# Performance work log

Hardware: AMD Instinct MI355X
Metric: run time of the kernel (lower is better)

The kernel has to match this reference:

```python
import jax, jax.numpy as jnp
import numpy as np
import math

B, Q, D, H = 256, 512, 32, 192
BLOCKS, KERNEL, EXPAND = 2, 9, 2
HID = H * EXPAND
IN_CH = 3 * D  # feature_mode='y_dy_ddy'


def _ln(x, w, b, eps=1e-5):
    m = x.mean(-1, keepdims=True)
    v = ((x - m) ** 2).mean(-1, keepdims=True)
    return (x - m) * jax.lax.rsqrt(v + eps) * w + b


def _features(x_in):
    # [y, dy, ddy] with dy[0]=0, ddy[0]=ddy[1 via diff]=...
    dy = jnp.concatenate([jnp.zeros_like(x_in[:, :1]), jnp.diff(x_in, axis=1)], axis=1)
    ddy = jnp.concatenate([jnp.zeros_like(dy[:, :1]), jnp.diff(dy, axis=1)], axis=1)
    return jnp.concatenate([x_in, dy, ddy], axis=-1)  # [B,Q,3D]


def _rotate(x, rho, phi):
    M = x.shape[-1] // 2
    re, im = x[:, :M], x[:, M:]
    c, s = jnp.cos(phi), jnp.sin(phi)
    return jnp.concatenate([rho * (c * re - s * im), rho * (s * re + c * im)], axis=1)


def _rho_phi(h2):
    return jax.nn.sigmoid(h2[:, 0:1]) * 1.25, math.pi * jnp.tanh(h2[:, 1:2])


def _block(h, dw_w, dw_b, ln_w, ln_b, pw1_w, pw1_b, grn_g, grn_b, pw2_w, pw2_b):
    # h: [B,C,T]; depthwise conv with replicate padding
    pad = KERNEL // 2
    y = jnp.pad(h, ((0, 0), (0, 0), (pad, pad)), mode='edge')
    y = jax.lax.conv_general_dilated(
        y, dw_w, (1,), 'VALID',
        dimension_numbers=('NCH', 'OIH', 'NCH'),
        feature_group_count=h.shape[1]) + dw_b[None, :, None]
    y = _ln(y.transpose(0, 2, 1), ln_w, ln_b).transpose(0, 2, 1)
    y = jnp.einsum('bct,oc->bot', y, pw1_w) + pw1_b[None, :, None]  # pw expand
    y = jax.nn.gelu(y, approximate=False)
    # GRN: L2 over time, normalize by channel-mean
    gx = jnp.sqrt(jnp.sum(y * y, axis=2, keepdims=True))  # [B,C,1]
    nx = gx / (gx.mean(axis=1, keepdims=True) + 1e-6)
    y = grn_g[None, :, None] * (y * nx) + grn_b[None, :, None] + y
    y = jnp.einsum('bct,oc->bot', y, pw2_w) + pw2_b[None, :, None]  # pw shrink
    return h + y  # dropout is identity in eval


def _forward(x_in, inp_w, inp_b, b_dw_w, b_dw_b, b_ln_w, b_ln_b,
             b_pw1_w, b_pw1_b, b_grn_g, b_grn_b, b_pw2_w, b_pw2_b,
             out_ln_w, out_ln_b, fc_rp_w, fc_rp_b, fc_gain_w, fc_gain_b,
             roll_in_w, roll_in_b, gru_wih, gru_whh, gru_bih, gru_bhh,
             roll_ln_w, roll_ln_b, fc_rp_r_w, fc_rp_r_b, w_out):
    feats = _features(x_in)  # [B,Q,3D]
    h = jnp.einsum('btc,oc->bot', feats, inp_w) + inp_b[None, :, None]  # [B,H,Q]
    for i in range(BLOCKS):
        h = _block(h, b_dw_w[i], b_dw_b[i], b_ln_w[i], b_ln_b[i],
                   b_pw1_w[i], b_pw1_b[i], b_grn_g[i], b_grn_b[i],
                   b_pw2_w[i], b_pw2_b[i])
    h_seq = _ln(h.transpose(0, 2, 1), out_ln_w, out_ln_b)  # [B,Q,H]

    # predict-correct Kalman loop (sequential over Q)
    def kstep(x_post, inp):
        h_t, y_t = inp
        rho, phi = _rho_phi(h_t @ fc_rp_w.T + fc_rp_b)
        x_pri = _rotate(x_post, rho, phi)
        gain = jax.nn.sigmoid(h_t @ fc_gain_w.T + fc_gain_b)
        return x_pri + gain * (y_t - x_pri), None

    x_post, _ = jax.lax.scan(
        kstep, x_in[:, 0, :],
        (h_seq.transpose(1, 0, 2), x_in.transpose(1, 0, 2)))

    # GRU rollout
    Hn = gru_whh.shape[1]

    def rstep(carry, _):
        h_r, curr = carry
        x = jnp.tanh(jnp.concatenate([h_r, curr], 1) @ roll_in_w.T + roll_in_b)
        gi = x @ gru_wih.T + gru_bih
        gh = h_r @ gru_whh.T + gru_bhh
        r = jax.nn.sigmoid(gi[:, :Hn] + gh[:, :Hn])
        z = jax.nn.sigmoid(gi[:, Hn:2 * Hn] + gh[:, Hn:2 * Hn])
        n = jnp.tanh(gi[:, 2 * Hn:] + r * gh[:, 2 * Hn:])
        h_new = _ln((1 - z) * n + z * h_r, roll_ln_w, roll_ln_b)
        rho, phi = _rho_phi(h_new @ fc_rp_r_w.T + fc_rp_r_b)
        curr_new = _rotate(curr, rho, phi)
        return (h_new, curr_new), curr_new

    _, preds = jax.lax.scan(rstep, (h_seq[:, -1, :], x_post), None, length=w_out)
    return preds.transpose(1, 0, 2)  # [B, w_out, D]


def setup_inputs() -> dict:
    key = jax.random.key(0)
    ks = jax.random.split(key, 32)
    n = lambda i, shape, s=0.05: jax.random.normal(ks[i], shape, jnp.float32) * s
    return {
        'x_in': jax.random.normal(ks[0], (B, Q, D), jnp.float32),
        'inp_w': n(1, (H, IN_CH)), 'inp_b': n(2, (H,)),
        'b_dw_w': n(3, (BLOCKS, H, 1, KERNEL)), 'b_dw_b': n(4, (BLOCKS, H)),
        'b_ln_w': 1.0 + n(5, (BLOCKS, H)), 'b_ln_b': n(6, (BLOCKS, H)),
        'b_pw1_w': n(7, (BLOCKS, HID, H)), 'b_pw1_b': n(8, (BLOCKS, HID)),
        'b_grn_g': n(9, (BLOCKS, HID)), 'b_grn_b': n(10, (BLOCKS, HID)),
        'b_pw2_w': n(11, (BLOCKS, H, HID)), 'b_pw2_b': n(12, (BLOCKS, H)),
        'out_ln_w': 1.0 + n(13, (H,)), 'out_ln_b': n(14, (H,)),
        'fc_rp_w': n(15, (2, H)), 'fc_rp_b': n(16, (2,)),
        'fc_gain_w': n(17, (D, H)), 'fc_gain_b': n(18, (D,)),
        'roll_in_w': n(19, (H, H + D)), 'roll_in_b': n(20, (H,)),
        'gru_wih': n(21, (3 * H, H)), 'gru_whh': n(22, (3 * H, H)),
        'gru_bih': n(23, (3 * H,)), 'gru_bhh': n(24, (3 * H,)),
        'roll_ln_w': 1.0 + n(25, (H,)), 'roll_ln_b': n(26, (H,)),
        'fc_rp_r_w': n(27, (2, H)), 'fc_rp_r_b': n(28, (2,)),
        'w_out': 64,
    }


def reference(x_in, inp_w, inp_b, b_dw_w, b_dw_b, b_ln_w, b_ln_b,
              b_pw1_w, b_pw1_b, b_grn_g, b_grn_b, b_pw2_w, b_pw2_b,
              out_ln_w, out_ln_b, fc_rp_w, fc_rp_b, fc_gain_w, fc_gain_b,
              roll_in_w, roll_in_b, gru_wih, gru_whh, gru_bih, gru_bhh,
              roll_ln_w, roll_ln_b, fc_rp_r_w, fc_rp_r_b, w_out):
    return _forward(x_in, inp_w, inp_b, b_dw_w, b_dw_b, b_ln_w, b_ln_b,
                    b_pw1_w, b_pw1_b, b_grn_g, b_grn_b, b_pw2_w, b_pw2_b,
                    out_ln_w, out_ln_b, fc_rp_w, fc_rp_b, fc_gain_w, fc_gain_b,
                    roll_in_w, roll_in_b, gru_wih, gru_whh, gru_bih, gru_bhh,
                    roll_ln_w, roll_ln_b, fc_rp_r_w, fc_rp_r_b, int(w_out))
```

## Files before the change

### kernel.cpp

```cpp
#include <hip/hip_runtime.h>
#include <cstdint>
#include <cstddef>

#define B_    256
#define Q_    512
#define D_    32
#define H_    192
#define HID_  384
#define INCH_ 96
#define M_    (B_*Q_)
#define WOUT_ 64
#define BPB   2
#define RT_   768
#define PI_F  3.14159265358979323846f
#define LDS_S 40

typedef unsigned int uint_t;
typedef __attribute__((ext_vector_type(8))) short short8v;
typedef __attribute__((ext_vector_type(4))) float floatx4;

__device__ __forceinline__ float sigm(float x){ return 1.f/(1.f+expf(-x)); }
__device__ __forceinline__ float gelu_exact(float x){ return 0.5f*x*(1.f+erff(x*0.7071067811865475f)); }
__device__ __forceinline__ float4 f4sub(float4 a, float4 b){
  return make_float4(a.x-b.x, a.y-b.y, a.z-b.z, a.w-b.w);
}

__device__ __forceinline__ void f2bf2(float v, unsigned short& h, unsigned short& l){
  unsigned u = __float_as_uint(v);
  unsigned rh = u + 0x7FFFu + ((u>>16)&1u);
  h = (unsigned short)(rh>>16);
  float fh = __uint_as_float(((unsigned)h)<<16);
  float lo = v - fh;
  unsigned ul = __float_as_uint(lo);
  unsigned rl = ul + 0x7FFFu + ((ul>>16)&1u);
  l = (unsigned short)(rl>>16);
}

#define MFMA_BF16(a,b,c) __builtin_amdgcn_mfma_f32_16x16x32_bf16((a),(b),(c),0,0,0)

__device__ __forceinline__ float4 feats_load(const float* __restrict__ x, int bt, int c){
  const int t = bt & 511;
  const int seg = c >> 5, d = c & 31;
  const float* xr = x + (size_t)bt*D_ + d;
  float4 x0 = *(const float4*)xr;
  if (seg == 0) return x0;
  if (t == 0) return make_float4(0.f,0.f,0.f,0.f);
  float4 x1 = *(const float4*)(xr - D_);
  float4 dy = f4sub(x0, x1);
  if (seg == 1) return dy;
  if (t == 1) return dy;
  float4 x2 = *(const float4*)(xr - 2*D_);
  float4 dym1 = f4sub(x1, x2);
  return f4sub(dy, dym1);
}

__global__ void prep_wbf_kernel(const float* __restrict__ w1, const float* __restrict__ w2,
                                unsigned short* __restrict__ w1h, unsigned short* __restrict__ w1l,
                                unsigned short* __restrict__ w2h, unsigned short* __restrict__ w2l)
{
  int idx = blockIdx.x*256 + threadIdx.x;
  const int n1 = 2*HID_*H_;
  if (idx < n1){
    unsigned short h,l; f2bf2(w1[idx],h,l);
    w1h[idx]=h; w1l[idx]=l;
    return;
  }
  idx -= n1;
  if (idx < 2*H_*HID_){
    unsigned short h,l; f2bf2(w2[idx],h,l);
    w2h[idx]=h; w2l[idx]=l;
  }
}

template<int MODE>
__global__ __launch_bounds__(256,2) void gemm_mfma(
    const float* __restrict__ Af, const unsigned* __restrict__ Ap,
    const unsigned short* __restrict__ Wh, const unsigned short* __restrict__ Wl,
    const float* __restrict__ bias,
    float* __restrict__ Cf,
    const float* __restrict__ scale, const float* __restrict__ grnb,
    float* __restrict__ gpart,
    int N, int K)
{
  __shared__ __align__(16) unsigned short smem[25600];
  unsigned short* Ah = smem;
  unsigned short* Al = smem + 128*LDS_S;
  unsigned short* Bh = smem + 256*LDS_S;
  unsigned short* Bl = smem + 256*LDS_S + 192*LDS_S;

  const int tid  = threadIdx.x;
  const int lane = tid & 63;
  const int wv   = tid >> 6;
  const int l15  = lane & 15;
  const int lg   = lane >> 4;
  const int bm = blockIdx.x*128, bn = blockIdx.y*192;

  floatx4 acc[2][12];
  #pragma unroll
  for (int i=0;i<2;i++)
    #pragma unroll
    for (int j=0;j<12;j++) acc[i][j] = (floatx4){0.f,0.f,0.f,0.f};

  const int arow = tid >> 1, akq = (tid & 1)*16;
  const float*    gA  = (MODE==2) ? (Af + (size_t)(bm+arow)*K) : nullptr;
  const unsigned* gAp = (MODE==1) ? (Ap + (size_t)(bm+arow)*K) : nullptr;
  const float* srow = (MODE==2) ? (scale + (size_t)(bm>>9)*HID_) : nullptr;

  for (int k0=0; k0<K; k0+=32){
    if (MODE==1){
      #pragma unroll
      for (int i=0;i<4;i++){
        uint4 u = *(const uint4*)(gAp + k0 + akq + 4*i);
        unsigned h01 = (u.x & 0xFFFFu) | (u.y << 16);
        unsigned h23 = (u.z & 0xFFFFu) | (u.w << 16);
        unsigned l01 = (u.x >> 16) | (u.y & 0xFFFF0000u);
        unsigned l23 = (u.z >> 16) | (u.w & 0xFFFF0000u);
        uint2 uh; uh.x=h01; uh.y=h23;
        uint2 ul; ul.x=l01; ul.y=l23;
        *(uint2*)&Ah[arow*LDS_S + akq + 4*i] = uh;
        *(uint2*)&Al[arow*LDS_S + akq + 4*i] = ul;
      }
    } else {
      #pragma unroll
      for (int i=0;i<4;i++){
        float4 v = *(const float4*)(gA + k0 + akq + 4*i);
        int c = k0 + akq + 4*i;
        float4 sc = *(const float4*)(srow+c);
        float4 gb = *(const float4*)(grnb+c);
        v.x = v.x*sc.x+gb.x; v.y = v.y*sc.y+gb.y;
        v.z = v.z*sc.z+gb.z; v.w = v.w*sc.w+gb.w;
        unsigned short h0,h1,h2,h3,l0,l1,l2,l3;
        f2bf2(v.x,h0,l0); f2bf2(v.y,h1,l1); f2bf2(v.z,h2,l2); f2bf2(v.w,h3,l3);
        uint2 uh; uh.x = (unsigned)h0 | ((unsigned)h1<<16); uh.y = (unsigned)h2 | ((unsigned)h3<<16);
        uint2 ul; ul.x = (unsigned)l0 | ((unsigned)l1<<16); ul.y = (unsigned)l2 | ((unsigned)l3<<16);
        *(uint2*)&Ah[arow*LDS_S + akq + 4*i] = uh;
        *(uint2*)&Al[arow*LDS_S + akq + 4*i] = ul;
      }
    }
    for (int idx = tid; idx < 384; idx += 256){
      int br = idx >> 1, bkq = (idx & 1)*16;
      const unsigned short* gh = Wh + (size_t)(bn+br)*K + k0 + bkq;
      const unsigned short* gl = Wl + (size_t)(bn+br)*K + k0 + bkq;
      uint4 vh0 = *(const uint4*)(gh);
      uint4 vh1 = *(const uint4*)(gh+8);
      uint4 vl0 = *(const uint4*)(gl);
      uint4 vl1 = *(const uint4*)(gl+8);
      *(uint4*)&Bh[br*LDS_S + bkq]     = vh0;
      *(uint4*)&Bh[br*LDS_S + bkq + 8] = vh1;
      *(uint4*)&Bl[br*LDS_S + bkq]     = vl0;
      *(uint4*)&Bl[br*LDS_S + bkq + 8] = vl1;
    }
    __syncthreads();

    const int a0off = (wv*32 + l15)*LDS_S + 8*lg;
    const int a1off = a0off + 16*LDS_S;
    short8v ah0 = *(const short8v*)&Ah[a0off];
    short8v al0 = *(const short8v*)&Al[a0off];
    short8v ah1 = *(const short8v*)&Ah[a1off];
    short8v al1 = *(const short8v*)&Al[a1off];
    #pragma unroll
    for (int ct=0; ct<12; ct++){
      const int boff = (ct*16 + l15)*LDS_S + 8*lg;
      short8v bh = *(const short8v*)&Bh[boff];
      short8v bl = *(const short8v*)&Bl[boff];
      acc[0][ct] = MFMA_BF16(ah0, bh, acc[0][ct]);
      acc[0][ct] = MFMA_BF16(ah0, bl, acc[0][ct]);
      acc[0][ct] = MFMA_BF16(al0, bh, acc[0][ct]);
      acc[1][ct] = MFMA_BF16(ah1, bh, acc[1][ct]);
      acc[1][ct] = MFMA_BF16(ah1, bl, acc[1][ct]);
      acc[1][ct] = MFMA_BF16(al1, bh, acc[1][ct]);
    }
    __syncthreads();
  }

  if (MODE==1){
    float* gq = (float*)smem;
    #pragma unroll
    for (int ct=0; ct<12; ct++){
      const int col = bn + ct*16 + l15;
      const float b = bias[col];
      float qc = 0.f;
      #pragma unroll
      for (int rt=0; rt<2; rt++){
        const int rbase = bm + wv*32 + rt*16 + lg*4;
        #pragma unroll
        for (int r=0;r<4;r++){
          float v = gelu_exact(acc[rt][ct][r] + b);
          Cf[(size_t)(rbase+r)*N + col] = v;
          qc += v*v;
        }
      }
      gq[(ct*16+l15)*16 + (wv*4+lg)] = qc;
    }
    __syncthreads();
    if (tid < 192){
      float s = 0.f;
      #pragma unroll
      for (int j=0;j<16;j++) s += gq[tid*16+j];
      const int slot = (bm>>7)&3, b = bm>>9;
      gpart[((size_t)(b*4+slot))*HID_ + bn + tid] = s;
    }
  } else {
    #pragma unroll
    for (int ct=0; ct<12; ct++){
      const int col = bn + ct*16 + l15;
      const float b = bias[col];
      #pragma unroll
      for (int rt=0; rt<2; rt++){
        const int rbase = bm + wv*32 + rt*16 + lg*4;
        #pragma unroll
        for (int r=0;r<4;r++){
          size_t off = (size_t)(rbase+r)*N + col;
          Cf[off] = Cf[off] + acc[rt][ct][r] + b;
        }
      }
    }
  }
}

__global__ __launch_bounds__(256,2) void gemm_inp_w192(
    const float* __restrict__ x,
    const float* __restrict__ W,  const float* __restrict__ bias,
    float* __restrict__ Cf)
{
  __shared__ float smem[16*128 + 16*192];
  float* AsB = smem;
  float* BsB = smem + 16*128;
  const int tid = threadIdx.x;
  const int bm = blockIdx.x*128;
  const int tx = tid & 15, ty = tid >> 4;
  const int arow = tid >> 1, ak = (tid & 1)*4;
  const int br = tid >> 2,  bk = (tid & 3)*4;
  const int K = INCH_, N = H_;

  float acc[8][12];
  #pragma unroll
  for (int i=0;i<8;i++)
    #pragma unroll
    for (int j=0;j<12;j++) acc[i][j]=0.f;

  const float* gB0 = W + (size_t)(br)*K;
  const float* gB1 = W + (size_t)(br+64)*K;
  const float* gB2 = W + (size_t)(br+128)*K;

  for (int k0=0;k0<K;k0+=16){
    float4 va0 = feats_load(x, bm+arow, k0+ak);
    float4 va1 = feats_load(x, bm+arow, k0+ak+8);
    float4 vb0 = *(const float4*)(gB0 + k0 + bk);
    float4 vb1 = *(const float4*)(gB1 + k0 + bk);
    float4 vb2 = *(const float4*)(gB2 + k0 + bk);
    AsB[(ak+0)*128+arow]=va0.x; AsB[(ak+1)*128+arow]=va0.y; AsB[(ak+2)*128+arow]=va0.z; AsB[(ak+3)*128+arow]=va0.w;
    AsB[(ak+8)*128+arow]=va1.x; AsB[(ak+9)*128+arow]=va1.y; AsB[(ak+10)*128+arow]=va1.z; AsB[(ak+11)*128+arow]=va1.w;
    BsB[(bk+0)*192+br]=vb0.x; BsB[(bk+1)*192+br]=vb0.y; BsB[(bk+2)*192+br]=vb0.z; BsB[(bk+3)*192+br]=vb0.w;
    BsB[(bk+0)*192+br+64]=vb1.x; BsB[(bk+1)*192+br+64]=vb1.y; BsB[(bk+2)*192+br+64]=vb1.z; BsB[(bk+3)*192+br+64]=vb1.w;
    BsB[(bk+0)*192+br+128]=vb2.x; BsB[(bk+1)*192+br+128]=vb2.y; BsB[(bk+2)*192+br+128]=vb2.z; BsB[(bk+3)*192+br+128]=vb2.w;
    __syncthreads();
    #pragma unroll
    for (int kk=0;kk<16;kk++){
      float4 a0 = *(const float4*)&AsB[kk*128 + ty*8];
      float4 a1 = *(const float4*)&AsB[kk*128 + ty*8 + 4];
      float4 b0 = *(const float4*)&BsB[kk*192 + tx*12];
      float4 b1 = *(const float4*)&BsB[kk*192 + tx*12 + 4];
      float4 b2 = *(const float4*)&BsB[kk*192 + tx*12 + 8];
      float ar[8] = {a0.x,a0.y,a0.z,a0.w,a1.x,a1.y,a1.z,a1.w};
      #pragma unroll
      for (int i=0;i<8;i++){
        acc[i][0] += ar[i]*b0.x; acc[i][1] += ar[i]*b0.y; acc[i][2] += ar[i]*b0.z; acc[i][3] += ar[i]*b0.w;
        acc[i][4] += ar[i]*b1.x; acc[i][5] += ar[i]*b1.y; acc[i][6] += ar[i]*b1.z; acc[i][7] += ar[i]*b1.w;
        acc[i][8] += ar[i]*b2.x; acc[i][9] += ar[i]*b2.y; acc[i][10]+= ar[i]*b2.z; acc[i][11]+= ar[i]*b2.w;
      }
    }
    __syncthreads();
  }

  const int o0 = tx*12;
  float4 bb0 = *(const float4*)(bias + o0);
  float4 bb1 = *(const float4*)(bias + o0 + 4);
  float4 bb2 = *(const float4*)(bias + o0 + 8);
  #pragma unroll
  for (int i=0;i<8;i++){
    int m = bm + ty*8 + i;
    float* crow = Cf + (size_t)m*N + o0;
    float4 v0, v1, v2;
    v0.x=acc[i][0]+bb0.x; v0.y=acc[i][1]+bb0.y; v0.z=acc[i][2]+bb0.z; v0.w=acc[i][3]+bb0.w;
    v1.x=acc[i][4]+bb1.x; v1.y=acc[i][5]+bb1.y; v1.z=acc[i][6]+bb1.z; v1.w=acc[i][7]+bb1.w;
    v2.x=acc[i][8]+bb2.x; v2.y=acc[i][9]+bb2.y; v2.z=acc[i][10]+bb2.z; v2.w=acc[i][11]+bb2.w;
    *(float4*)(crow+0) = v0; *(float4*)(crow+4) = v1; *(float4*)(crow+8) = v2;
  }
}

template<int MODE>
__global__ __launch_bounds__(256,4) void gemm_t128(
    const float* __restrict__ Af,
    const float* __restrict__ W,  const float* __restrict__ bias,
    float* __restrict__ Cf,
    const float* __restrict__ scale, const float* __restrict__ grnb,
    float* __restrict__ gpart,
    int N, int K)
{
  __shared__ float As[16][128];
  __shared__ float Bs[16][64];
  const int tid = threadIdx.x;
  const int bm = blockIdx.x*128, bn = blockIdx.y*64;
  const int tx = tid & 15, ty = tid >> 4;
  const int arow = tid >> 1, ak = (tid & 1)*4;
  const int brow = tid >> 2, bk = (tid & 3)*4;

  float acc[8][4];
  #pragma unroll
  for (int i=0;i<8;i++)
    #pragma unroll
    for (int j=0;j<4;j++) acc[i][j]=0.f;

  const float* gA = Af + (size_t)(bm+arow)*K;
  const float* gB = W  + (size_t)(bn+brow)*K;

  for (int k0=0;k0<K;k0+=16){
    float4 va0 = *(const float4*)(gA + k0 + ak);
    float4 va1 = *(const float4*)(gA + k0 + ak + 8);
    float4 vb  = *(const float4*)(gB + k0 + bk);
    As[ak+0][arow]=va0.x; As[ak+1][arow]=va0.y; As[ak+2][arow]=va0.z; As[ak+3][arow]=va0.w;
    As[ak+8][arow]=va1.x; As[ak+9][arow]=va1.y; As[ak+10][arow]=va1.z; As[ak+11][arow]=va1.w;
    Bs[bk+0][brow]=vb.x; Bs[bk+1][brow]=vb.y; Bs[bk+2][brow]=vb.z; Bs[bk+3][brow]=vb.w;
    __syncthreads();
    #pragma unroll
    for (int kk=0;kk<16;kk++){
      float4 a0 = *(const float4*)&As[kk][ty*8];
      float4 a1 = *(const float4*)&As[kk][ty*8+4];
      float4 b  = *(const float4*)&Bs[kk][tx*4];
      float ar[8] = {a0.x,a0.y,a0.z,a0.w,a1.x,a1.y,a1.z,a1.w};
      #pragma unroll
      for (int i=0;i<8;i++){
        acc[i][0] += ar[i]*b.x; acc[i][1] += ar[i]*b.y;
        acc[i][2] += ar[i]*b.z; acc[i][3] += ar[i]*b.w;
      }
    }
    __syncthreads();
  }

  const int o0 = bn + tx*4;
  float4 b0 = *(const float4*)(bias + o0);

  if (MODE==3){
    #pragma unroll
    for (int i=0;i<8;i++){
      int m = bm + ty*8 + i;
      float* ob = Cf + (size_t)m*34;
      float vx = acc[i][0]+b0.x, vy = acc[i][1]+b0.y;
      float vz = acc[i][2]+b0.z, vw = acc[i][3]+b0.w;
      if (o0 == 0){
        float rho = 1.25f*sigm(vx);
        float phi = PI_F*tanhf(vy);
        ob[0] = rho*cosf(phi); ob[1] = rho*sinf(phi);
        ob[2] = sigm(vz); ob[3] = sigm(vw);
      } else if (o0 <= 28){
        ob[o0+0]=sigm(vx); ob[o0+1]=sigm(vy); ob[o0+2]=sigm(vz); ob[o0+3]=sigm(vw);
      } else if (o0 == 32){
        ob[32]=sigm(vx); ob[33]=sigm(vy);
      }
    }
    return;
  }
  (void)gpart; (void)scale; (void)grnb;
}

__global__ __launch_bounds__(256) void dwconv_ln_wave(
  const float* __restrict__ h, const float* __restrict__ dww, const float* __restrict__ dwb,
  const float* __restrict__ lnw, const float* __restrict__ lnb, unsigned* __restrict__ yln)
{
  __shared__ float sh[24][192];
  const int tid  = threadIdx.x;
  const int lane = tid & 63;
  const int wv   = tid >> 6;
  const int t0 = (blockIdx.x & 31) * 16;
  const size_t base = (size_t)(blockIdx.x >> 5) * Q_ * H_;
  #pragma unroll
  for (int i = tid; i < 24*192; i += 256){
    int r = i / 192, c = i - r*192;
    int tt = t0 - 4 + r; tt = tt<0?0:(tt>511?511:tt);
    sh[r][c] = h[base + (size_t)tt*H_ + c];
  }
  const int c0 = lane, c1 = lane+64, c2 = lane+128;
  float w0[9], w1[9], w2[9];
  #pragma unroll
  for (int k=0;k<9;k++){ w0[k]=dww[c0*9+k]; w1[k]=dww[c1*9+k]; w2[k]=dww[c2*9+k]; }
  const float db0=dwb[c0], db1=dwb[c1], db2=dwb[c2];
  const float lw0=lnw[c0], lw1=lnw[c1], lw2=lnw[c2];
  const float lb0=lnb[c0], lb1=lnb[c1], lb2=lnb[c2];
  __syncthreads();
  for (int it=0; it<4; it++){
    const int i = it*4 + wv;
    float a0=db0, a1=db1, a2=db2;
    #pragma unroll
    for (int k=0;k<9;k++){
      a0 += w0[k]*sh[i+k][c0];
      a1 += w1[k]*sh[i+k][c1];
      a2 += w2[k]*sh[i+k][c2];
    }
    float s = a0+a1+a2;
    float qq = a0*a0 + a1*a1 + a2*a2;
    #pragma unroll
    for (int off=32; off>0; off>>=1){ s += __shfl_down(s,off); qq += __shfl_down(qq,off); }
    s = __shfl(s, 0); qq = __shfl(qq, 0);
    float mean = s*(1.f/H_);
    float var  = qq*(1.f/H_) - mean*mean;
    float r = rsqrtf(var + 1e-5f);
    unsigned* ob = yln + base + (size_t)(t0+i)*H_;
    unsigned short hh,ll;
    f2bf2((a0-mean)*r*lw0 + lb0, hh, ll); ob[c0] = (unsigned)hh | ((unsigned)ll<<16);
    f2bf2((a1-mean)*r*lw1 + lb1, hh, ll); ob[c1] = (unsigned)hh | ((unsigned)ll<<16);
    f2bf2((a2-mean)*r*lw2 + lb2, hh, ll); ob[c2] = (unsigned)hh | ((unsigned)ll<<16);
  }
}

__global__ __launch_bounds__(256) void out_ln_wave(
  const float* __restrict__ h, const float* __restrict__ lnw, const float* __restrict__ lnb,
  float* __restrict__ o, float* __restrict__ hlast, int b0)
{
  const int tid  = threadIdx.x;
  const int lane = tid & 63;
  const int wv   = tid >> 6;
  const int bt = blockIdx.x*4 + wv;
  const float* hr = h + (size_t)bt*H_;
  float v0 = hr[lane], v1 = hr[lane+64], v2 = hr[lane+128];
  float s = v0+v1+v2;
  float qq = v0*v0 + v1*v1 + v2*v2;
  #pragma unroll
  for (int off=32; off>0; off>>=1){ s += __shfl_down(s,off); qq += __shfl_down(qq,off); }
  s = __shfl(s, 0); qq = __shfl(qq, 0);
  float mean = s*(1.f/H_);
  float var  = qq*(1.f/H_) - mean*mean;
  float r = rsqrtf(var + 1e-5f);
  const float r0 = (v0-mean)*r*lnw[lane]     + lnb[lane];
  const float r1 = (v1-mean)*r*lnw[lane+64]  + lnb[lane+64];
  const float r2 = (v2-mean)*r*lnw[lane+128] + lnb[lane+128];
  float* orow = o + (size_t)bt*H_;
  orow[lane] = r0; orow[lane+64] = r1; orow[lane+128] = r2;
  if ((bt & 511) == 511){
    float* hl = hlast + (size_t)(b0 + (bt>>9))*H_;
    hl[lane] = r0; hl[lane+64] = r1; hl[lane+128] = r2;
  }
}

__global__ __launch_bounds__(384) void grn_combine_kernel(
  const float* __restrict__ gpart, const float* __restrict__ grn_g, float* __restrict__ scale)
{
  __shared__ float r[384];
  const int c = threadIdx.x;
  const int b = blockIdx.x;
  const float* p = gpart + (size_t)b*4*HID_;
  float s = ((p[c] + p[HID_+c]) + p[2*HID_+c]) + p[3*HID_+c];
  float gx = sqrtf(s);
  r[c] = gx;
  __syncthreads();
  if (c < 64){
    float v = r[c]+r[c+64]+r[c+128]+r[c+192]+r[c+256]+r[c+320];
    #pragma unroll
    for (int off=32; off>0; off>>=1) v += __shfl_down(v,off);
    if (c==0) r[0]=v;
  }
  __syncthreads();
  float mean = r[0]*(1.f/HID_);
  scale[(size_t)b*HID_ + c] = 1.f + grn_g[c]*gx/(mean + 1e-6f);
}

__global__ void pack_w_kernel(const float* __restrict__ frw, const float* __restrict__ frb,
                              const float* __restrict__ fgw, const float* __restrict__ fgb,
                              float* __restrict__ w_pad, float* __restrict__ b_pad)
{
  int idx = blockIdx.x*256 + threadIdx.x;
  if (idx >= 64*192) return;
  int o = idx / 192, k = idx % 192;
  float v = 0.f;
  if (o < 2) v = frw[o*192+k]; else if (o < 34) v = fgw[(o-2)*192+k];
  w_pad[idx] = v;
  if (k == 0){
    float bv = 0.f;
    if (o < 2) bv = frb[o]; else if (o < 34) bv = fgb[o-2];
    b_pad[o] = bv;
  }
}

__global__ __launch_bounds__(64) void kalman_scan_kernel(
  const float* __restrict__ x_c, const float* __restrict__ rp, float* __restrict__ xpost,
  int b0, int Bc)
{
  const int lane = threadIdx.x;
  const int bl = blockIdx.x*4 + (lane>>4);
  if (bl >= Bc) return;
  const int m = lane & 15;
  const float* xb  = x_c + (size_t)bl*Q_*D_;
  const float* rpb = rp  + (size_t)bl*Q_*34;
  float re = xb[m], im = xb[16+m];
  for (int t=0;t<Q_;t++){
    const float* r = rpb + (size_t)t*34;
    float rc = r[0], rs = r[1];
    float g0 = r[2+m], g1 = r[18+m];
    float y0 = xb[(size_t)t*D_ + m], y1v = xb[(size_t)t*D_ + 16 + m];
    float pr  = rc*re - rs*im;
    float pim = rs*re + rc*im;
    re = pr  + g0*(y0  - pr);
    im = pim + g1*(y1v - pim);
  }
  xpost[(b0+bl)*D_ + m] = re;
  xpost[(b0+bl)*D_ + 16 + m] = im;
}

__global__ void prep_rollout_kernel(const float* __restrict__ riw, const float* __restrict__ wih,
                                    const float* __restrict__ whh,
                                    float* __restrict__ wT1, float* __restrict__ wPack)
{
  int idx = blockIdx.x*256 + threadIdx.x;
  if (idx < 224*192){
    int o = idx % 192, k = idx / 192;
    wT1[idx] = riw[o*224 + k];
    return;
  }
  idx -= 224*192;
  if (idx < 192*192){
    int o = idx % 192, k = idx / 192;
    float* w = wPack + ((size_t)(k>>1)*192 + o)*12 + (k&1)*6;
    w[0] = wih[(0*192+o)*192 + k];
    w[1] = wih[(1*192+o)*192 + k];
    w[2] = wih[(2*192+o)*192 + k];
    w[3] = whh[(0*192+o)*192 + k];
    w[4] = whh[(1*192+o)*192 + k];
    w[5] = whh[(2*192+o)*192 + k];
  }
}

__global__ __launch_bounds__(RT_,3) void rollout_kernel(
  const float* __restrict__ hlast, const float* __restrict__ xpost,
  const float* __restrict__ wT1,  const float* __restrict__ rib_,
  const float* __restrict__ wPack,
  const float* __restrict__ bih,  const float* __restrict__ bhh,
  const float* __restrict__ lnw,  const float* __restrict__ lnb,
  const float* __restrict__ frw,  const float* __restrict__ frb,
  float* __restrict__ out)
{
  const int tid = threadIdx.x;
  const int q   = tid / 192;
  const int o   = tid - q*192;
  const int bb  = blockIdx.x*BPB;

  __shared__ float hT[192][2];
  __shared__ float xT[192][2];
  __shared__ float cT[32][2];
  __shared__ float pA[4][2][192];
  __shared__ float pB[4][12][192];
  __shared__ float rsum[2][3][4];

  if (q < 2){
    hT[o][q] = hlast[(size_t)(bb+q)*H_ + o];
    if (o < 32) cT[o][q] = xpost[(bb+q)*D_ + o];
  }

  const float w_ln = lnw[o], b_ln = lnb[o];
  const float fr0  = frw[o], fr1  = frw[192+o];
  const float fb0 = frb[0],  fb1 = frb[1];
  const float bi0 = bih[o], bi1 = bih[192+o], bi2 = bih[384+o];
  const float bh0 = bhh[o], bh1 = bhh[192+o], bh2 = bhh[384+o];
  const float rib = rib_[o];
  const float u0 = w_ln*fr0, u1 = w_ln*fr1;
  const float t0c = b_ln*fr0, t1c = b_ln*fr1;

  float wreg[56];
  if (q < 3){
    const int kb = 56*q;
    #pragma unroll
    for (int i=0;i<56;i++) wreg[i] = wT1[(kb+i)*192+o];
  } else {
    #pragma unroll
    for (int i=0;i<24;i++) wreg[i] = wT1[(168+i)*192+o];
    #pragma unroll
    for (int i=0;i<32;i++) wreg[24+i] = wT1[(192+i)*192+o];
  }

  {
    float c0=u0, c1=u1, k0=t0c, k1=t1c;
    #pragma unroll
    for (int off=32; off>0; off>>=1){
      c0 += __shfl_down(c0,off); c1 += __shfl_down(c1,off);
      k0 += __shfl_down(k0,off); k1 += __shfl_down(k1,off);
    }
    if (q==0 && (o&63)==0){
      int w = o>>6;
      rsum[0][w][0]=c0; rsum[0][w][1]=c1; rsum[0][w][2]=k0; rsum[0][w][3]=k1;
    }
  }
  __syncthreads();
  const float C0 = rsum[0][0][0]+rsum[0][1][0]+rsum[0][2][0];
  const float C1 = rsum[0][0][1]+rsum[0][1][1]+rsum[0][2][1];
  const float K0 = rsum[0][0][2]+rsum[0][1][2]+rsum[0][2][2] + fb0;
  const float K1 = rsum[0][0][3]+rsum[0][1][3]+rsum[0][2][3] + fb1;

  for (int s=0; s<WOUT_; s++){
    float a0=0.f, a1=0.f;
    if (q < 3){
      const int kb = 56*q;
      #pragma unroll
      for (int i=0;i<56;i++){
        float2 h2 = *(const float2*)&hT[kb+i][0];
        a0 += wreg[i]*h2.x; a1 += wreg[i]*h2.y;
      }
    } else {
      #pragma unroll
      for (int i=0;i<24;i++){
        float2 h2 = *(const float2*)&hT[168+i][0];
        a0 += wreg[i]*h2.x; a1 += wreg[i]*h2.y;
      }
      #pragma unroll
      for (int i=0;i<32;i++){
        float2 c2 = *(const float2*)&cT[i][0];
        a0 += wreg[24+i]*c2.x; a1 += wreg[24+i]*c2.y;
      }
    }
    pA[q][0][o]=a0; pA[q][1][o]=a1;
    __syncthreads();

    if (q < 2){
      xT[o][q] = tanhf(rib + pA[0][q][o] + pA[1][q][o] + pA[2][q][o] + pA[3][q][o]);
    }
    __syncthreads();

    float accx[2][3] = {{0.f,0.f,0.f},{0.f,0.f,0.f}};
    float acch[2][3] = {{0.f,0.f,0.f},{0.f,0.f,0.f}};
    {
      const int pb = 24*q;
      #pragma unroll 2
      for (int i=0;i<24;i++){
        const int p = pb+i;
        const float4* wp = (const float4*)(wPack + ((size_t)p*192 + o)*12);
        const float4 qa = wp[0];
        const float4 qb = wp[1];
        const float4 qc = wp[2];
        const float4 xx = *(const float4*)&xT[2*p][0];
        const float4 hh = *(const float4*)&hT[2*p][0];
        accx[0][0] += qa.x*xx.x; accx[0][1] += qa.y*xx.x; accx[0][2] += qa.z*xx.x;
        accx[1][0] += qa.x*xx.y; accx[1][1] += qa.y*xx.y; accx[1][2] += qa.z*xx.y;
        acch[0][0] += qa.w*hh.x; acch[0][1] += qb.x*hh.x; acch[0][2] += qb.y*hh.x;
        acch[1][0] += qa.w*hh.y; acch[1][1] += qb.x*hh.y; acch[1][2] += qb.y*hh.y;
        accx[0][0] += qb.z*xx.z; accx[0][1] += qb.w*xx.z; accx[0][2] += qc.x*xx.z;
        accx[1][0] += qb.z*xx.w; accx[1][1] += qb.w*xx.w; accx[1][2] += qc.x*xx.w;
        acch[0][0] += qc.y*hh.z; acch[0][1] += qc.z*hh.z; acch[0][2] += qc.w*hh.z;
        acch[1][0] += qc.y*hh.w; acch[1][1] += qc.z*hh.w; acch[1][2] += qc.w*hh.w;
      }
    }
    #pragma unroll
    for (int j=0;j<2;j++){
      #pragma unroll
      for (int g=0;g<3;g++){
        pB[q][j*6+g][o]   = accx[j][g];
        pB[q][j*6+3+g][o] = acch[j][g];
      }
    }
    __syncthreads();

    float pre = 0.f;
    if (q < 2){
      const int g6 = q*6;
      float P0 = bi0 + pB[0][g6+0][o]+pB[1][g6+0][o]+pB[2][g6+0][o]+pB[3][g6+0][o];
      float P1 = bi1 + pB[0][g6+1][o]+pB[1][g6+1][o]+pB[2][g6+1][o]+pB[3][g6+1][o];
      float P2 = bi2 + pB[0][g6+2][o]+pB[1][g6+2][o]+pB[2][g6+2][o]+pB[3][g6+2][o];
      float Q0 = bh0 + pB[0][g6+3][o]+pB[1][g6+3][o]+pB[2][g6+3][o]+pB[3][g6+3][o];
      float Q1 = bh1 + pB[0][g6+4][o]+pB[1][g6+4][o]+pB[2][g6+4][o]+pB[3][g6+4][o];
      float Q2 = bh2 + pB[0][g6+5][o]+pB[1][g6+5][o]+pB[2][g6+5][o]+pB[3][g6+5][o];
      float rg = sigm(P0+Q0), zz = sigm(P1+Q1);
      float nn = tanhf(P2 + rg*Q2);
      pre = (1.f-zz)*nn + zz*hT[o][q];
      float s1 = pre, s2 = pre*pre, s3 = pre*u0, s4 = pre*u1;
      #pragma unroll
      for (int off=32; off>0; off>>=1){
        s1 += __shfl_down(s1,off); s2 += __shfl_down(s2,off);
        s3 += __shfl_down(s3,off); s4 += __shfl_down(s4,off);
      }
      if ((o&63)==0){
        int w = o>>6;
        rsum[q][w][0]=s1; rsum[q][w][1]=s2; rsum[q][w][2]=s3; rsum[q][w][3]=s4;
      }
    }
    __syncthreads();

    if (q < 2){
      float S1 = rsum[q][0][0]+rsum[q][1][0]+rsum[q][2][0];
      float S2 = rsum[q][0][1]+rsum[q][1][1]+rsum[q][2][1];
      float mu  = S1*(1.f/192.f);
      float var = S2*(1.f/192.f) - mu*mu;
      float r = rsqrtf(var+1e-5f);
      hT[o][q] = (pre-mu)*r*w_ln + b_ln;
    } else if (o < 16){
      const int j = q-2;
      float S1 = rsum[j][0][0]+rsum[j][1][0]+rsum[j][2][0];
      float S2 = rsum[j][0][1]+rsum[j][1][1]+rsum[j][2][1];
      float S3 = rsum[j][0][2]+rsum[j][1][2]+rsum[j][2][2];
      float S4 = rsum[j][0][3]+rsum[j][1][3]+rsum[j][2][3];
      float mu  = S1*(1.f/192.f);
      float var = S2*(1.f/192.f) - mu*mu;
      float r = rsqrtf(var+1e-5f);
      float proj0 = r*(S3 - mu*C0) + K0;
      float proj1 = r*(S4 - mu*C1) + K1;
      float rho = 1.25f*sigm(proj0);
      float phi = PI_F*tanhf(proj1);
      float rc = rho*cosf(phi), rs = rho*sinf(phi);
      float re = cT[o][j], im = cT[o+16][j];
      float nre = rc*re - rs*im;
      float nim = rs*re + rc*im;
      cT[o][j] = nre; cT[o+16][j] = nim;
      float* ob = out + ((size_t)(bb+j)*WOUT_ + s)*D_;
      ob[o] = nre; ob[o+16] = nim;
    }
    __syncthreads();
  }
}

extern "C" void kernel_launch(void* const* d_in, const int* in_sizes, int n_in,
                              void* d_out, int out_size, void* d_ws, size_t ws_size,
                              hipStream_t stream)
{
  const float* x_in     = (const float*)d_in[0];
  const float* inp_w    = (const float*)d_in[1];
  const float* inp_b    = (const float*)d_in[2];
  const float* b_dw_w   = (const float*)d_in[3];
  const float* b_dw_b   = (const float*)d_in[4];
  const float* b_ln_w   = (const float*)d_in[5];
  const float* b_ln_b   = (const float*)d_in[6];
  const float* b_pw1_w  = (const float*)d_in[7];
  const float* b_pw1_b  = (const float*)d_in[8];
  const float* b_grn_g  = (const float*)d_in[9];
  const float* b_grn_b  = (const float*)d_in[10];
  const float* b_pw2_w  = (const float*)d_in[11];
  const float* b_pw2_b  = (const float*)d_in[12];
  const float* out_ln_w = (const float*)d_in[13];
  const float* out_ln_b = (const float*)d_in[14];
  const float* fc_rp_w  = (const float*)d_in[15];
  const float* fc_rp_b  = (const float*)d_in[16];
  const float* fc_gain_w= (const float*)d_in[17];
  const float* fc_gain_b= (const float*)d_in[18];
  const float* roll_in_w= (const float*)d_in[19];
  const float* roll_in_b= (const float*)d_in[20];
  const float* gru_wih  = (const float*)d_in[21];
  const float* gru_whh  = (const float*)d_in[22];
  const float* gru_bih  = (const float*)d_in[23];
  const float* gru_bhh  = (const float*)d_in[24];
  const float* roll_ln_w= (const float*)d_in[25];
  const float* roll_ln_b= (const float*)d_in[26];
  const float* fc_rp_r_w= (const float*)d_in[27];
  const float* fc_rp_r_b= (const float*)d_in[28];
  float* out = (float*)d_out;

  const size_t SMAL_FLOATS = 1194048 + 4096;
  size_t ws_floats = ws_size / 4;
  int nchunk = 256;
  const int cand[9] = {1,2,4,8,16,32,64,128,256};
  for (int ci=0; ci<9; ci++){
    size_t Mc_try = (size_t)M_ / cand[ci];
    if (Mc_try*768 + SMAL_FLOATS <= ws_floats){ nchunk = cand[ci]; break; }
  }
  const int    Bc = B_ / nchunk;
  const size_t Mc = (size_t)Bc * Q_;

  float* ws    = (float*)d_ws;
  float* h_c   = ws;
  float* yln_c = h_c   + Mc*192;
  float* mid_c = yln_c + Mc*192;
  float* smal  = mid_c + Mc*384;

  float* y1_c    = mid_c;
  float* rp_c    = mid_c;

  float* scaleB = smal;
  float* w_pad  = smal + 98304;
  float* b_pad  = w_pad + 12288;
  float* xpost  = b_pad + 64;
  float* hlast  = xpost + 8192;
  float* wT1    = hlast + 49152;
  float* wPack  = wT1 + 43008;
  float* gpart  = wPack + 294912;
  float* wbf    = gpart + 393216;
  unsigned short* w1h = (unsigned short*)wbf;
  unsigned short* w1l = w1h + 2*HID_*H_;
  unsigned short* w2h = w1l + 2*HID_*H_;
  unsigned short* w2l = w2h + 2*H_*HID_;

  pack_w_kernel<<<(64*192+255)/256, 256, 0, stream>>>(fc_rp_w, fc_rp_b, fc_gain_w, fc_gain_b, w_pad, b_pad);
  prep_rollout_kernel<<<(224*192+192*192+255)/256, 256, 0, stream>>>(roll_in_w, gru_wih, gru_whh, wT1, wPack);
  prep_wbf_kernel<<<(4*HID_*H_+255)/256, 256, 0, stream>>>(b_pw1_w, b_pw2_w, w1h, w1l, w2h, w2l);

  const int gmx = (int)(Mc/128);
  for (int ch=0; ch<nchunk; ch++){
    const float* x_c = x_in + (size_t)ch*Mc*D_;
    gemm_inp_w192<<<dim3(gmx, 1), 256, 0, stream>>>(x_c, inp_w, inp_b, h_c);
    for (int blk = 0; blk < 2; blk++){
      const float* dww = b_dw_w + blk*H_*9;     const float* dwb = b_dw_b + blk*H_;
      const float* lnw = b_ln_w + blk*H_;       const float* lnb = b_ln_b + blk*H_;
      const float* p1b = b_pw1_b + blk*HID_;
      const float* gg  = b_grn_g + blk*HID_;    const float* gb  = b_grn_b + blk*HID_;
      const float* p2b = b_pw2_b + blk*H_;
      dwconv_ln_wave<<<(int)(Mc/16), 256, 0, stream>>>(h_c, dww, dwb, lnw, lnb, (unsigned*)yln_c);
      gemm_mfma<1><<<dim3(gmx, 2), 256, 0, stream>>>(nullptr, (const unsigned*)yln_c,
                                                     w1h + blk*HID_*H_, w1l + blk*HID_*H_, p1b,
                                                     y1_c, nullptr, nullptr, gpart, HID_, H_);
      grn_combine_kernel<<<Bc, 384, 0, stream>>>(gpart, gg, scaleB);
      gemm_mfma<2><<<dim3(gmx, 1), 256, 0, stream>>>(y1_c, nullptr,
                                                     w2h + blk*H_*HID_, w2l + blk*H_*HID_, p2b,
                                                     h_c, scaleB, gb, nullptr, H_, HID_);
    }
    out_ln_wave<<<(int)(Mc/4), 256, 0, stream>>>(h_c, out_ln_w, out_ln_b, yln_c, hlast, ch*Bc);
    gemm_t128<3><<<dim3(gmx, 1), 256, 0, stream>>>(yln_c, w_pad, b_pad,
                                                   rp_c, nullptr, nullptr, nullptr, 64, H_);
    kalman_scan_kernel<<<(Bc+3)/4, 64, 0, stream>>>(x_c, rp_c, xpost, ch*Bc, Bc);
  }
  rollout_kernel<<<B_/BPB, RT_, 0, stream>>>(hlast, xpost, wT1, roll_in_b, wPack,
                                             gru_bih, gru_bhh, roll_ln_w, roll_ln_b,
                                             fc_rp_r_w, fc_rp_r_b, out);
  (void)in_sizes; (void)n_in; (void)out_size; (void)ws_size;
}
```

Baseline: 1.889 ms.

## Move output projection to MFMA, fuse GRN combine, widen dwconv tile

Replaces the fp32 SIMT projection GEMM with a bf16 hi/lo split MFMA kernel. To feed it, the output LayerNorm now writes packed bf16 pairs and the projection weights are converted once up front. The GRN scale computation is folded into the start of the second pointwise GEMM, removing a launch and a global round trip. The depthwise conv tile grows from 16 to 32 timesteps per block, which cuts halo reloads but halves the grid. Together these aim to reduce launch count and fp32 FMA work, at the cost of redundant per-block GRN reductions and three-product bf16 approximation error.

```diff
diff --git a/kernel.cpp b/kernel.cpp
--- a/kernel.cpp
+++ b/kernel.cpp
@@ -72,17 +72,27 @@
   }
 }
 
+__global__ void prep_wpad_bf(const float* __restrict__ wp,
+                             unsigned short* __restrict__ ph, unsigned short* __restrict__ pl)
+{
+  int idx = blockIdx.x*256 + threadIdx.x;
+  if (idx >= 64*192) return;
+  unsigned short h,l; f2bf2(wp[idx],h,l);
+  ph[idx]=h; pl[idx]=l;
+}
+
 template<int MODE>
 __global__ __launch_bounds__(256,2) void gemm_mfma(
     const float* __restrict__ Af, const unsigned* __restrict__ Ap,
     const unsigned short* __restrict__ Wh, const unsigned short* __restrict__ Wl,
     const float* __restrict__ bias,
     float* __restrict__ Cf,
-    const float* __restrict__ scale, const float* __restrict__ grnb,
+    const float* __restrict__ grn_g, const float* __restrict__ grnb,
     float* __restrict__ gpart,
     int N, int K)
 {
   __shared__ __align__(16) unsigned short smem[25600];
+  __shared__ float scLDS[HID_];
   unsigned short* Ah = smem;
   unsigned short* Al = smem + 128*LDS_S;
   unsigned short* Bh = smem + 256*LDS_S;
@@ -95,6 +105,29 @@
   const int lg   = lane >> 4;
   const int bm = blockIdx.x*128, bn = blockIdx.y*192;
 
+  if (MODE==2){
+    float* gx = (float*)smem;
+    const int b = bm>>9;
+    const float* p = gpart + (size_t)b*4*HID_;
+    for (int c=tid; c<HID_; c+=256){
+      float s = ((p[c] + p[HID_+c]) + p[2*HID_+c]) + p[3*HID_+c];
+      gx[c] = sqrtf(s);
+    }
+    __syncthreads();
+    if (tid < 64){
+      float v = gx[tid]+gx[tid+64]+gx[tid+128]+gx[tid+192]+gx[tid+256]+gx[tid+320];
+      #pragma unroll
+      for (int off=32; off>0; off>>=1) v += __shfl_down(v,off);
+      if (tid==0) gx[400] = v;
+    }
+    __syncthreads();
+    const float mean = gx[400]*(1.f/HID_);
+    for (int c=tid; c<HID_; c+=256){
+      scLDS[c] = 1.f + grn_g[c]*gx[c]/(mean + 1e-6f);
+    }
+    __syncthreads();
+  }
+
   floatx4 acc[2][12];
   #pragma unroll
   for (int i=0;i<2;i++)
@@ -104,7 +137,6 @@
   const int arow = tid >> 1, akq = (tid & 1)*16;
   const float*    gA  = (MODE==2) ? (Af + (size_t)(bm+arow)*K) : nullptr;
   const unsigned* gAp = (MODE==1) ? (Ap + (size_t)(bm+arow)*K) : nullptr;
-  const float* srow = (MODE==2) ? (scale + (size_t)(bm>>9)*HID_) : nullptr;
 
   for (int k0=0; k0<K; k0+=32){
     if (MODE==1){
@@ -125,7 +157,7 @@
       for (int i=0;i<4;i++){
         float4 v = *(const float4*)(gA + k0 + akq + 4*i);
         int c = k0 + akq + 4*i;
-        float4 sc = *(const float4*)(srow+c);
+        float4 sc = *(const float4*)&scLDS[c];
         float4 gb = *(const float4*)(grnb+c);
         v.x = v.x*sc.x+gb.x; v.y = v.y*sc.y+gb.y;
         v.z = v.z*sc.z+gb.z; v.w = v.w*sc.w+gb.w;
@@ -212,6 +244,113 @@
         for (int r=0;r<4;r++){
           size_t off = (size_t)(rbase+r)*N + col;
           Cf[off] = Cf[off] + acc[rt][ct][r] + b;
+        }
+      }
+    }
+  }
+}
+
+__global__ __launch_bounds__(256,2) void gemm_mfma_proj(
+    const unsigned* __restrict__ Ap,
+    const unsigned short* __restrict__ Wh, const unsigned short* __restrict__ Wl,
+    const float* __restrict__ bias,
+    float* __restrict__ rp)
+{
+  __shared__ __align__(16) unsigned short smem[15360];
+  unsigned short* Ah = smem;
+  unsigned short* Al = smem + 128*LDS_S;
+  unsigned short* Bh = smem + 256*LDS_S;
+  unsigned short* Bl = smem + 256*LDS_S + 64*LDS_S;
+  const int K = H_;
+
+  const int tid  = threadIdx.x;
+  const int lane = tid & 63;
+  const int wv   = tid >> 6;
+  const int l15  = lane & 15;
+  const int lg   = lane >> 4;
+  const int bm = blockIdx.x*128;
+
+  floatx4 acc[2][4];
+  #pragma unroll
+  for (int i=0;i<2;i++)
+    #pragma unroll
+    for (int j=0;j<4;j++) acc[i][j] = (floatx4){0.f,0.f,0.f,0.f};
+
+  const int arow = tid >> 1, akq = (tid & 1)*16;
+  const unsigned* gAp = Ap + (size_t)(bm+arow)*K;
+
+  for (int k0=0; k0<K; k0+=32){
+    #pragma unroll
+    for (int i=0;i<4;i++){
+      uint4 u = *(const uint4*)(gAp + k0 + akq + 4*i);
+      unsigned h01 = (u.x & 0xFFFFu) | (u.y << 16);
+      unsigned h23 = (u.z & 0xFFFFu) | (u.w << 16);
+      unsigned l01 = (u.x >> 16) | (u.y & 0xFFFF0000u);
+      unsigned l23 = (u.z >> 16) | (u.w & 0xFFFF0000u);
+      uint2 uh; uh.x=h01; uh.y=h23;
+      uint2 ul; ul.x=l01; ul.y=l23;
+      *(uint2*)&Ah[arow*LDS_S + akq + 4*i] = uh;
+      *(uint2*)&Al[arow*LDS_S + akq + 4*i] = ul;
+    }
+    if (tid < 128){
+      int br = tid >> 1, bkq = (tid & 1)*16;
+      const unsigned short* gh = Wh + (size_t)br*K + k0 + bkq;
+      const unsigned short* gl = Wl + (size_t)br*K + k0 + bkq;
+      uint4 vh0 = *(const uint4*)(gh);
+      uint4 vh1 = *(const uint4*)(gh+8);
+      uint4 vl0 = *(const uint4*)(gl);
+      uint4 vl1 = *(const uint4*)(gl+8);
+      *(uint4*)&Bh[br*LDS_S + bkq]     = vh0;
+      *(uint4*)&Bh[br*LDS_S + bkq + 8] = vh1;
+      *(uint4*)&Bl[br*LDS_S + bkq]     = vl0;
+      *(uint4*)&Bl[br*LDS_S + bkq + 8] = vl1;
+    }
+    __syncthreads();
+
+    const int a0off = (wv*32 + l15)*LDS_S + 8*lg;
+    const int a1off = a0off + 16*LDS_S;
+    short8v ah0 = *(const short8v*)&Ah[a0off];
+    short8v al0 = *(const short8v*)&Al[a0off];
+    short8v ah1 = *(const short8v*)&Ah[a1off];
+    short8v al1 = *(const short8v*)&Al[a1off];
+    #pragma unroll
+    for (int ct=0; ct<4; ct++){
+      const int boff = (ct*16 + l15)*LDS_S + 8*lg;
+      short8v bh = *(const short8v*)&Bh[boff];
+      short8v bl = *(const short8v*)&Bl[boff];
+      acc[0][ct] = MFMA_BF16(ah0, bh, acc[0][ct]);
+      acc[0][ct] = MFMA_BF16(ah0, bl, acc[0][ct]);
+      acc[0][ct] = MFMA_BF16(al0, bh, acc[0][ct]);
+      acc[1][ct] = MFMA_BF16(ah1, bh, acc[1][ct]);
+      acc[1][ct] = MFMA_BF16(ah1, bl, acc[1][ct]);
+      acc[1][ct] = MFMA_BF16(al1, bh, acc[1][ct]);
+    }
+    __syncthreads();
+  }
+
+  #pragma unroll
+  for (int ct=0; ct<4; ct++){
+    const int c = ct*16 + l15;
+    const float b = bias[c];
+    #pragma unroll
+    for (int rt=0; rt<2; rt++){
+      const int rbase = bm + wv*32 + rt*16 + lg*4;
+      #pragma unroll
+      for (int r=0;r<4;r++){
+        float val = acc[rt][ct][r] + b;
+        float* ob = rp + (size_t)(rbase+r)*34;
+        if (ct == 0){
+          float vn = __shfl(val, lane+1);
+          if (l15 == 0){
+            float rho = 1.25f*sigm(val);
+            float phi = PI_F*tanhf(vn);
+            ob[0] = rho*cosf(phi);
+            ob[1] = rho*sinf(phi);
+          } else if (c >= 2){
+            ob[c] = sigm(val);
+          }
+        } else if (c <= 33){
+          ob[c] = sigm(val);
         }
       }
     }
@@ -289,93 +428,17 @@
   }
 }
 
-template<int MODE>
-__global__ __launch_bounds__(256,4) void gemm_t128(
-    const float* __restrict__ Af,
-    const float* __restrict__ W,  const float* __restrict__ bias,
-    float* __restrict__ Cf,
-    const float* __restrict__ scale, const float* __restrict__ grnb,
-    float* __restrict__ gpart,
-    int N, int K)
-{
-  __shared__ float As[16][128];
-  __shared__ float Bs[16][64];
-  const int tid = threadIdx.x;
-  const int bm = blockIdx.x*128, bn = blockIdx.y*64;
-  const int tx = tid & 15, ty = tid >> 4;
-  const int arow = tid >> 1, ak = (tid & 1)*4;
-  const int brow = tid >> 2, bk = (tid & 3)*4;
-
-  float acc[8][4];
-  #pragma unroll
-  for (int i=0;i<8;i++)
-    #pragma unroll
-    for (int j=0;j<4;j++) acc[i][j]=0.f;
-
-  const float* gA = Af + (size_t)(bm+arow)*K;
-  const float* gB = W  + (size_t)(bn+brow)*K;
-
-  for (int k0=0;k0<K;k0+=16){
-    float4 va0 = *(const float4*)(gA + k0 + ak);
-    float4 va1 = *(const float4*)(gA + k0 + ak + 8);
-    float4 vb  = *(const float4*)(gB + k0 + bk);
-    As[ak+0][arow]=va0.x; As[ak+1][arow]=va0.y; As[ak+2][arow]=va0.z; As[ak+3][arow]=va0.w;
-    As[ak+8][arow]=va1.x; As[ak+9][arow]=va1.y; As[ak+10][arow]=va1.z; As[ak+11][arow]=va1.w;
-    Bs[bk+0][brow]=vb.x; Bs[bk+1][brow]=vb.y; Bs[bk+2][brow]=vb.z; Bs[bk+3][brow]=vb.w;
-    __syncthreads();
-    #pragma unroll
-    for (int kk=0;kk<16;kk++){
-      float4 a0 = *(const float4*)&As[kk][ty*8];
-      float4 a1 = *(const float4*)&As[kk][ty*8+4];
-      float4 b  = *(const float4*)&Bs[kk][tx*4];
-      float ar[8] = {a0.x,a0.y,a0.z,a0.w,a1.x,a1.y,a1.z,a1.w};
-      #pragma unroll
-      for (int i=0;i<8;i++){
-        acc[i][0] += ar[i]*b.x; acc[i][1] += ar[i]*b.y;
-        acc[i][2] += ar[i]*b.z; acc[i][3] += ar[i]*b.w;
-      }
-    }
-    __syncthreads();
-  }
-
-  const int o0 = bn + tx*4;
-  float4 b0 = *(const float4*)(bias + o0);
-
-  if (MODE==3){
-    #pragma unroll
-    for (int i=0;i<8;i++){
-      int m = bm + ty*8 + i;
-      float* ob = Cf + (size_t)m*34;
-      float vx = acc[i][0]+b0.x, vy = acc[i][1]+b0.y;
-      float vz = acc[i][2]+b0.z, vw = acc[i][3]+b0.w;
-      if (o0 == 0){
-        float rho = 1.25f*sigm(vx);
-        float phi = PI_F*tanhf(vy);
-        ob[0] = rho*cosf(phi); ob[1] = rho*sinf(phi);
-        ob[2] = sigm(vz); ob[3] = sigm(vw);
-      } else if (o0 <= 28){
-        ob[o0+0]=sigm(vx); ob[o0+1]=sigm(vy); ob[o0+2]=sigm(vz); ob[o0+3]=sigm(vw);
-      } else if (o0 == 32){
-        ob[32]=sigm(vx); ob[33]=sigm(vy);
-      }
-    }
-    return;
-  }
-  (void)gpart; (void)scale; (void)grnb;
-}
-
 __global__ __launch_bounds__(256) void dwconv_ln_wave(
   const float* __restrict__ h, const float* __restrict__ dww, const float* __restrict__ dwb,
   const float* __restrict__ lnw, const float* __restrict__ lnb, unsigned* __restrict__ yln)
 {
-  __shared__ float sh[24][192];
+  __shared__ float sh[40][192];
   const int tid  = threadIdx.x;
   const int lane = tid & 63;
   const int wv   = tid >> 6;
-  const int t0 = (blockIdx.x & 31) * 16;
-  const size_t base = (size_t)(blockIdx.x >> 5) * Q_ * H_;
-  #pragma unroll
-  for (int i = tid; i < 24*192; i += 256){
+  const int t0 = (blockIdx.x & 15) * 32;
+  const size_t base = (size_t)(blockIdx.x >> 4) * Q_ * H_;
+  for (int i = tid; i < 40*192; i += 256){
     int r = i / 192, c = i - r*192;
     int tt = t0 - 4 + r; tt = tt<0?0:(tt>511?511:tt);
     sh[r][c] = h[base + (size_t)tt*H_ + c];
@@ -388,7 +451,7 @@
   const float lw0=lnw[c0], lw1=lnw[c1], lw2=lnw[c2];
   const float lb0=lnb[c0], lb1=lnb[c1], lb2=lnb[c2];
   __syncthreads();
-  for (int it=0; it<4; it++){
+  for (int it=0; it<8; it++){
     const int i = it*4 + wv;
     float a0=db0, a1=db1, a2=db2;
     #pragma unroll
@@ -415,7 +478,7 @@
 
 __global__ __launch_bounds__(256) void out_ln_wave(
   const float* __restrict__ h, const float* __restrict__ lnw, const float* __restrict__ lnb,
-  float* __restrict__ o, float* __restrict__ hlast, int b0)
+  unsigned* __restrict__ o, float* __restrict__ hlast, int b0)
 {
   const int tid  = threadIdx.x;
   const int lane = tid & 63;
@@ -434,34 +497,15 @@
   const float r0 = (v0-mean)*r*lnw[lane]     + lnb[lane];
   const float r1 = (v1-mean)*r*lnw[lane+64]  + lnb[lane+64];
   const float r2 = (v2-mean)*r*lnw[lane+128] + lnb[lane+128];
-  float* orow = o + (size_t)bt*H_;
-  orow[lane] = r0; orow[lane+64] = r1; orow[lane+128] = r2;
+  unsigned* orow = o + (size_t)bt*H_;
+  unsigned short hh,ll;
+  f2bf2(r0,hh,ll); orow[lane]     = (unsigned)hh | ((unsigned)ll<<16);
+  f2bf2(r1,hh,ll); orow[lane+64]  = (unsigned)hh | ((unsigned)ll<<16);
+  f2bf2(r2,hh,ll); orow[lane+128] = (unsigned)hh | ((unsigned)ll<<16);
   if ((bt & 511) == 511){
     float* hl = hlast + (size_t)(b0 + (bt>>9))*H_;
     hl[lane] = r0; hl[lane+64] = r1; hl[lane+128] = r2;
   }
-}
-
-__global__ __launch_bounds__(384) void grn_combine_kernel(
-  const float* __restrict__ gpart, const float* __restrict__ grn_g, float* __restrict__ scale)
-{
-  __shared__ float r[384];
-  const int c = threadIdx.x;
-  const int b = blockIdx.x;
-  const float* p = gpart + (size_t)b*4*HID_;
-  float s = ((p[c] + p[HID_+c]) + p[2*HID_+c]) + p[3*HID_+c];
-  float gx = sqrtf(s);
-  r[c] = gx;
-  __syncthreads();
-  if (c < 64){
-    float v = r[c]+r[c+64]+r[c+128]+r[c+192]+r[c+256]+r[c+320];
-    #pragma unroll
-    for (int off=32; off>0; off>>=1) v += __shfl_down(v,off);
-    if (c==0) r[0]=v;
-  }
-  __syncthreads();
-  float mean = r[0]*(1.f/HID_);
-  scale[(size_t)b*HID_ + c] = 1.f + grn_g[c]*gx/(mean + 1e-6f);
 }
 
 __global__ void pack_w_kernel(const float* __restrict__ frw, const float* __restrict__ frb,
@@ -748,7 +792,7 @@
   const float* fc_rp_r_b= (const float*)d_in[28];
   float* out = (float*)d_out;
 
-  const size_t SMAL_FLOATS = 1194048 + 4096;
+  const size_t SMAL_FLOATS = 1206336 + 4096;
   size_t ws_floats = ws_size / 4;
   int nchunk = 256;
   const int cand[9] = {1,2,4,8,16,32,64,128,256};
@@ -781,10 +825,14 @@
   unsigned short* w1l = w1h + 2*HID_*H_;
   unsigned short* w2h = w1l + 2*HID_*H_;
   unsigned short* w2l = w2h + 2*H_*HID_;
+  unsigned short* wph = w2l + 2*H_*HID_;
+  unsigned short* wpl = wph + 64*H_;
+  (void)scaleB;
 
   pack_w_kernel<<<(64*192+255)/256, 256, 0, stream>>>(fc_rp_w, fc_rp_b, fc_gain_w, fc_gain_b, w_pad, b_pad);
   prep_rollout_kernel<<<(224*192+192*192+255)/256, 256, 0, stream>>>(roll_in_w, gru_wih, gru_whh, wT1, wPack);
   prep_wbf_kernel<<<(4*HID_*H_+255)/256, 256, 0, stream>>>(b_pw1_w, b_pw2_w, w1h, w1l, w2h, w2l);
+  prep_wpad_bf<<<(64*192+255)/256, 256, 0, stream>>>(w_pad, wph, wpl);
 
   const int gmx = (int)(Mc/128);
   for (int ch=0; ch<nchunk; ch++){
@@ -796,18 +844,16 @@
       const float* p1b = b_pw1_b + blk*HID_;
       const float* gg  = b_grn_g + blk*HID_;    const float* gb  = b_grn_b + blk*HID_;
       const float* p2b = b_pw2_b + blk*H_;
-      dwconv_ln_wave<<<(int)(Mc/16), 256, 0, stream>>>(h_c, dww, dwb, lnw, lnb, (unsigned*)yln_c);
+      dwconv_ln_wave<<<(int)(Mc/32), 256, 0, stream>>>(h_c, dww, dwb, lnw, lnb, (unsigned*)yln_c);
       gemm_mfma<1><<<dim3(gmx, 2), 256, 0, stream>>>(nullptr, (const unsigned*)yln_c,
                                                      w1h + blk*HID_*H_, w1l + blk*HID_*H_, p1b,
                                                      y1_c, nullptr, nullptr, gpart, HID_, H_);
-      grn_combine_kernel<<<Bc, 384, 0, stream>>>(gpart, gg, scaleB);
       gemm_mfma<2><<<dim3(gmx, 1), 256, 0, stream>>>(y1_c, nullptr,
                                                      w2h + blk*H_*HID_, w2l + blk*H_*HID_, p2b,
-                                                     h_c, scaleB, gb, nullptr, H_, HID_);
-    }
-    out_ln_wave<<<(int)(Mc/4), 256, 0, stream>>>(h_c, out_ln_w, out_ln_b, yln_c, hlast, ch*Bc);
-    gemm_t128<3><<<dim3(gmx, 1), 256, 0, stream>>>(yln_c, w_pad, b_pad,
-                                                   rp_c, nullptr, nullptr, nullptr, 64, H_);
+                                                     h_c, gg, gb, gpart, H_, HID_);
+    }
+    out_ln_wave<<<(int)(Mc/4), 256, 0, stream>>>(h_c, out_ln_w, out_ln_b, (unsigned*)yln_c, hlast, ch*Bc);
+    gemm_mfma_proj<<<gmx, 256, 0, stream>>>((const unsigned*)yln_c, wph, wpl, b_pad, rp_c);
     kalman_scan_kernel<<<(Bc+3)/4, 64, 0, stream>>>(x_c, rp_c, xpost, ch*Bc, Bc);
   }
   rollout_kernel<<<B_/BPB, RT_, 0, stream>>>(hlast, xpost, wT1, roll_in_b, wPack,
```

Measured after the change: 1.888 ms. About the same (-0.0%).
